# Kernel optimization log

Hardware: AMD Instinct MI355X
Metric: run time of the kernel (lower is better)

The kernel has to match this reference:

```python
import jax, jax.numpy as jnp
import numpy as np
from jax import lax

C = 64      # embed_dim
DI = 128    # d_inner (expand=2)
N = 16      # d_state
RK = 4      # dt_rank = ceil(C/16)
K = 4       # scan directions
NB = 8      # total VSS blocks (4 stages x 2)


def conv2d(x, w, b, stride=1, pad=1, groups=1):
    y = lax.conv_general_dilated(x, w, (stride, stride), [(pad, pad), (pad, pad)],
                                 dimension_numbers=('NCHW', 'OIHW', 'NCHW'),
                                 feature_group_count=groups)
    return y + b[None, :, None, None]


def ln2d(x, g, b, eps=1e-6):
    xt = x.transpose(0, 2, 3, 1)
    mu = xt.mean(-1, keepdims=True)
    var = ((xt - mu) ** 2).mean(-1, keepdims=True)
    y = (xt - mu) / jnp.sqrt(var + eps) * g + b
    return y.transpose(0, 3, 1, 2)


def selective_scan(u, delta, A, Bm, Cm, D):
    # u, delta: (B,K,d,L); A: (K,d,n); Bm, Cm: (B,K,n,L); D: (K,d)
    dA = jnp.exp(delta[..., None] * A[None, :, :, None, :])               # (B,K,d,L,n)
    dBu = delta[..., None] * Bm.transpose(0, 1, 3, 2)[:, :, None] * u[..., None]

    def comb(c1, c2):
        a1, b1 = c1
        a2, b2 = c2
        return a2 * a1, a2 * b1 + b2

    _, h = lax.associative_scan(comb, (dA, dBu), axis=3)                  # (B,K,d,L,n)
    y = jnp.einsum('bkdln,bkln->bkdl', h, Cm.transpose(0, 1, 3, 2))
    return y + D[None, :, :, None] * u


def vss_block(x, lg, lb, inw, cw, cb, xpw, dtw, dtb, a_log, dp, ong, onb, outw):
    B, _, H, W = x.shape
    L = H * W
    h = ln2d(x, lg, lb)
    xz = jnp.einsum('bchw,ce->behw', h, inw)                              # (B,2*DI,H,W)
    xc, z = xz[:, :DI], xz[:, DI:]
    xc = jax.nn.silu(conv2d(xc, cw, cb, groups=DI))                       # depthwise 3x3
    x1 = xc.reshape(B, DI, L)                                             # row-major
    x2 = xc.transpose(0, 1, 3, 2).reshape(B, DI, L)                       # col-major
    xs = jnp.stack([x1, x2, x1[..., ::-1], x2[..., ::-1]], axis=1)        # (B,K,DI,L)
    xdbl = jnp.einsum('bkdl,krd->bkrl', xs, xpw)
    dts, Bs, Cs = xdbl[:, :, :RK], xdbl[:, :, RK:RK + N], xdbl[:, :, RK + N:]
    delta = jax.nn.softplus(jnp.einsum('bkrl,kdr->bkdl', dts, dtw) + dtb[None, :, :, None])
    A = -jnp.exp(a_log)
    ys = selective_scan(xs, delta, A, Bs, Cs, dp)                         # (B,K,DI,L)
    y = (ys[:, 0].reshape(B, DI, H, W)
         + ys[:, 1].reshape(B, DI, W, H).transpose(0, 1, 3, 2)
         + ys[:, 2, :, ::-1].reshape(B, DI, H, W)
         + ys[:, 3, :, ::-1].reshape(B, DI, W, H).transpose(0, 1, 3, 2))
    yt = y.transpose(0, 2, 3, 1)
    mu = yt.mean(-1, keepdims=True)
    var = ((yt - mu) ** 2).mean(-1, keepdims=True)
    yt = (yt - mu) / jnp.sqrt(var + 1e-6) * ong + onb
    yt = yt * jax.nn.silu(z.transpose(0, 2, 3, 1))
    out = jnp.einsum('bhwd,dc->bhwc', yt, outw).transpose(0, 3, 1, 2)
    return x + out


def setup_inputs() -> dict:
    key = jax.random.key(0)
    ks = jax.random.split(key, 16)
    nrm = lambda k, s, sc=0.02: jax.random.normal(k, s, jnp.float32) * sc
    return dict(
        E0=jax.random.uniform(ks[0], (1, 1, 256, 256), jnp.float32),
        pe_w=nrm(ks[1], (C, 1, 4, 4), 0.1),
        pe_b=jnp.zeros((C,), jnp.float32),
        pe_lg=jnp.ones((C,), jnp.float32),
        pe_lb=jnp.zeros((C,), jnp.float32),
        ln_g=jnp.ones((NB, C), jnp.float32),
        ln_b=jnp.zeros((NB, C), jnp.float32),
        in_w=nrm(ks[2], (NB, C, 2 * DI)),
        cv_w=nrm(ks[3], (NB, DI, 1, 3, 3), 0.1),
        cv_b=jnp.zeros((NB, DI), jnp.float32),
        xp_w=nrm(ks[4], (NB, K, RK + 2 * N, DI)),
        dt_w=nrm(ks[5], (NB, K, DI, RK)),
        dt_b=nrm(ks[6], (NB, K, DI), 0.5),
        A_log=jnp.broadcast_to(jnp.log(jnp.arange(1., N + 1)), (NB, K, DI, N)).astype(jnp.float32),
        Dp=jnp.ones((NB, K, DI), jnp.float32),
        on_g=jnp.ones((NB, DI), jnp.float32),
        on_b=jnp.zeros((NB, DI), jnp.float32),
        out_pw=nrm(ks[7], (NB, DI, C)),
        dn_w=nrm(ks[8], (3, C, C, 3, 3), 0.05),
        dn_b=jnp.zeros((3, C), jnp.float32),
        dn_g=jnp.ones((3, C), jnp.float32),
        dn_lb=jnp.zeros((3, C), jnp.float32),
        up_w=nrm(ks[9], (3, C, C, 3, 3), 0.05),
        up_b=jnp.zeros((3, C), jnp.float32),
        oc_w=nrm(ks[10], (C, C, 3, 3), 0.05),
        oc_b=jnp.zeros((C,), jnp.float32),
    )


def reference(E0, pe_w, pe_b, pe_lg, pe_lb, ln_g, ln_b, in_w, cv_w, cv_b, xp_w,
              dt_w, dt_b, A_log, Dp, on_g, on_b, out_pw, dn_w, dn_b, dn_g, dn_lb,
              up_w, up_b, oc_w, oc_b):
    x = conv2d(E0, pe_w, pe_b, stride=4, pad=0)
    x = ln2d(x, pe_lg, pe_lb)
    skips = []
    cur = 0
    for i in range(4):
        for _ in range(2):
            x = vss_block(x, ln_g[cur], ln_b[cur], in_w[cur], cv_w[cur], cv_b[cur],
                          xp_w[cur], dt_w[cur], dt_b[cur], A_log[cur], Dp[cur],
                          on_g[cur], on_b[cur], out_pw[cur])
            cur += 1
        skips.append(x)
        if i < 3:
            x = ln2d(conv2d(x, dn_w[i], dn_b[i], stride=2), dn_g[i], dn_lb[i])
    for i in range(3):
        Bq, Cq, Hq, Wq = x.shape
        x = jax.image.resize(x, (Bq, Cq, Hq * 2, Wq * 2), method='bilinear')
        x = jax.nn.silu(conv2d(x, up_w[i], up_b[i]))
        x = x + skips[-(i + 2)]
    Bq, Cq, Hq, Wq = x.shape
    x = jax.image.resize(x, (Bq, Cq, Hq * 4, Wq * 4), method='bilinear')
    x = jax.nn.silu(conv2d(x, oc_w, oc_b))
    return x
```

## Files before the change

### kernel.cpp

```cpp
#include <hip/hip_runtime.h>
#include <hip/hip_bf16.h>
#include <utility>

__global__ void k_patch_embed_ln(const float* __restrict__ E0, const float* __restrict__ w,
                                 const float* __restrict__ b, const float* __restrict__ g,
                                 const float* __restrict__ lb, float* __restrict__ out) {
  int p = blockIdx.x;
  int c = threadIdx.x;
  int oh = p >> 6, ow = p & 63;
  const float* src = E0 + (oh * 4) * 256 + ow * 4;
  const float* wc = w + c * 16;
  float acc = b[c];
#pragma unroll
  for (int i = 0; i < 4; i++)
#pragma unroll
    for (int j = 0; j < 4; j++) acc += src[i * 256 + j] * wc[i * 4 + j];
  float s = acc, s2 = acc * acc;
#pragma unroll
  for (int m = 32; m >= 1; m >>= 1) {
    s += __shfl_xor(s, m, 64);
    s2 += __shfl_xor(s2, m, 64);
  }
  float mu = s * (1.f / 64.f);
  float var = s2 * (1.f / 64.f) - mu * mu;
  float rstd = rsqrtf(var + 1e-6f);
  out[c * 4096 + p] = (acc - mu) * rstd * g[c] + lb[c];
}

__global__ void k_ln2d64(const float* __restrict__ x, const float* __restrict__ g,
                         const float* __restrict__ b, float* __restrict__ y, int HW) {
  int p = blockIdx.x;
  int c = threadIdx.x;
  float v = x[c * HW + p];
  float s = v, s2 = v * v;
#pragma unroll
  for (int m = 32; m >= 1; m >>= 1) {
    s += __shfl_xor(s, m, 64);
    s2 += __shfl_xor(s2, m, 64);
  }
  float mu = s * (1.f / 64.f);
  float var = s2 * (1.f / 64.f) - mu * mu;
  float rstd = rsqrtf(var + 1e-6f);
  y[c * HW + p] = (v - mu) * rstd * g[c] + b[c];
}

__global__ void k_lnproj(const float* __restrict__ x, const float* __restrict__ g,
                         const float* __restrict__ b, const float* __restrict__ w,
                         float* __restrict__ xc, float* __restrict__ z, int HW) {
  int p = blockIdx.x;
  int t = threadIdx.x;
  __shared__ float hsh[64];
  if (t < 64) {
    float v = x[t * HW + p];
    float s = v, s2 = v * v;
#pragma unroll
    for (int m = 32; m >= 1; m >>= 1) {
      s += __shfl_xor(s, m, 64);
      s2 += __shfl_xor(s2, m, 64);
    }
    float mu = s * (1.f / 64.f);
    float var = s2 * (1.f / 64.f) - mu * mu;
    float rstd = rsqrtf(var + 1e-6f);
    hsh[t] = (v - mu) * rstd * g[t] + b[t];
  }
  __syncthreads();
  float acc = 0.f;
  const float* wp = w + t;
#pragma unroll
  for (int c = 0; c < 64; c++) acc += hsh[c] * wp[c * 256];
  if (t < 128)
    xc[(size_t)p * 128 + t] = acc;
  else
    z[(size_t)p * 128 + (t - 128)] = acc;
}

__global__ void k_dwconv(const float* __restrict__ xc, const float* __restrict__ w,
                         const float* __restrict__ b, float* __restrict__ out, int H, int lgH) {
  int HW = H * H;
  int idx = blockIdx.x * blockDim.x + threadIdx.x;
  if (idx >= 128 * HW) return;
  int p = idx >> 7;
  int d = idx & 127;
  int ph = p >> lgH, pw = p & (H - 1);
  const float* wp = w + d * 9;
  float acc = b[d];
#pragma unroll
  for (int i = 0; i < 3; i++) {
    int ih = ph + i - 1;
    if (ih < 0 || ih >= H) continue;
#pragma unroll
    for (int j = 0; j < 3; j++) {
      int iw = pw + j - 1;
      if (iw < 0 || iw >= H) continue;
      acc += xc[(size_t)(ih * H + iw) * 128 + d] * wp[i * 3 + j];
    }
  }
  out[(size_t)p * 128 + d] = acc / (1.f + __expf(-acc));
}

__global__ void __launch_bounds__(256) k_xproj_scanA(
    const float* __restrict__ xcs, const float* __restrict__ xpw,
    const float* __restrict__ dtw, const float* __restrict__ dtb,
    const float* __restrict__ A_log, float* __restrict__ delta, float* __restrict__ Bs,
    float* __restrict__ Cs, float* __restrict__ hloc, float* __restrict__ pA, int H,
    int lgH, int nc, int cs) {
  int L = H * H;
  int c = blockIdx.x;
  int k = blockIdx.y;
  int t = threadIdx.x;
  int l0 = c * cs;
  __shared__ float xs[32][128];
  __shared__ float dsh[32][128];
  __shared__ float Bsh[32][16];
  __shared__ float r4s[4];
  for (int i = t; i < cs * 128; i += 256) {
    int j = i >> 7, d = i & 127;
    int l = l0 + j;
    int lm = (k & 2) ? (L - 1 - l) : l;
    int idx = (k & 1) ? ((lm & (H - 1)) * H + (lm >> lgH)) : lm;
    xs[j][d] = xcs[(size_t)idx * 128 + d];
  }
  int r = t >> 2, q = t & 3;
  float4 wreg[8];
  if (t < 144) {
    const float4* wp = (const float4*)(xpw + (size_t)(k * 36 + r) * 128 + q * 32);
#pragma unroll
    for (int m = 0; m < 8; m++) wreg[m] = wp[m];
  }
  float4 dtw4 = {0, 0, 0, 0};
  float dtbv = 0.f;
  if (t < 128) {
    dtw4 = *(const float4*)(dtw + (size_t)(k * 128 + t) * 4);
    dtbv = dtb[k * 128 + t];
  }
  __syncthreads();
  for (int j = 0; j < cs; j++) {
    if (t < 144) {
      const float4* xp = (const float4*)&xs[j][q * 32];
      float a = 0.f;
#pragma unroll
      for (int m = 0; m < 8; m++) {
        float4 xv = xp[m];
        a += xv.x * wreg[m].x + xv.y * wreg[m].y + xv.z * wreg[m].z + xv.w * wreg[m].w;
      }
      a += __shfl_xor(a, 1);
      a += __shfl_xor(a, 2);
      if (q == 0) {
        int l = l0 + j;
        if (r < 4)
          r4s[r] = a;
        else if (r < 20) {
          Bsh[j][r - 4] = a;
          Bs[((size_t)k * L + l) * 16 + (r - 4)] = a;
        } else
          Cs[((size_t)k * L + l) * 16 + (r - 20)] = a;
      }
    }
    __syncthreads();
    if (t < 128) {
      float dt = dtbv + r4s[0] * dtw4.x + r4s[1] * dtw4.y + r4s[2] * dtw4.z + r4s[3] * dtw4.w;
      float sp = fmaxf(dt, 0.f) + log1pf(__expf(-fabsf(dt)));
      dsh[j][t] = sp;
      delta[((size_t)k * L + (l0 + j)) * 128 + t] = sp;
    }
    __syncthreads();
  }
  if (t < 128) {
    int d = t;
    float A[16], h[16];
#pragma unroll
    for (int n = 0; n < 16; n++) {
      A[n] = -__expf(A_log[(size_t)(k * 128 + d) * 16 + n]);
      h[n] = 0.f;
    }
    float sumdt = 0.f;
    for (int j = 0; j < cs; j++) {
      float u = xs[j][d];
      float dt = dsh[j][d];
      float du = dt * u;
      sumdt += dt;
      const float4* bp = (const float4*)Bsh[j];
      float4 B0 = bp[0], B1 = bp[1], B2 = bp[2], B3 = bp[3];
      float Bv[16] = {B0.x, B0.y, B0.z, B0.w, B1.x, B1.y, B1.z, B1.w,
                      B2.x, B2.y, B2.z, B2.w, B3.x, B3.y, B3.z, B3.w};
#pragma unroll
      for (int n = 0; n < 16; n++) h[n] = __expf(dt * A[n]) * h[n] + Bv[n] * du;
    }
    size_t base = (((size_t)(k * 128 + d)) * nc + c) * 16;
#pragma unroll
    for (int n = 0; n < 16; n++) {
      hloc[base + n] = h[n];
      pA[base + n] = __expf(A[n] * sumdt);
    }
  }
}

__global__ void k_scanB(const float* __restrict__ hloc, const float* __restrict__ pA,
                        float* __restrict__ hinit, int nc) {
  int tid = blockIdx.x * blockDim.x + threadIdx.x;
  int k = tid >> 11;
  int d = (tid >> 4) & 127;
  int n = tid & 15;
  size_t rb = ((size_t)(k * 128 + d)) * nc * 16 + n;
  float h = 0.f;
  for (int c = 0; c < nc; c++) {
    size_t a = rb + (size_t)c * 16;
    hinit[a] = h;
    h = pA[a] * h + hloc[a];
  }
}

__global__ void k_scanC(const float* __restrict__ xcs, const float* __restrict__ delta,
                        const float* __restrict__ Bs, const float* __restrict__ Cs,
                        const float* __restrict__ A_log, const float* __restrict__ Dp,
                        const float* __restrict__ hinit, float* __restrict__ ys, int H,
                        int lgH, int nc, int cs) {
  int L = H * H;
  int c = blockIdx.x;
  int k = blockIdx.y;
  int d = threadIdx.x;
  float A[16], h[16];
  size_t base = (((size_t)(k * 128 + d)) * nc + c) * 16;
#pragma unroll
  for (int n = 0; n < 16; n++) {
    A[n] = -__expf(A_log[(size_t)(k * 128 + d) * 16 + n]);
    h[n] = hinit[base + n];
  }
  float Dv = Dp[k * 128 + d];
  int l0 = c * cs;
  for (int l = l0; l < l0 + cs; l++) {
    int lm = (k & 2) ? (L - 1 - l) : l;
    int idx = (k & 1) ? ((lm & (H - 1)) * H + (lm >> lgH)) : lm;
    float u = xcs[(size_t)idx * 128 + d];
    float dt = delta[((size_t)k * L + l) * 128 + d];
    float du = dt * u;
    const float4* bp = (const float4*)(Bs + ((size_t)k * L + l) * 16);
    float4 B0 = bp[0], B1 = bp[1], B2 = bp[2], B3 = bp[3];
    float Bv[16] = {B0.x, B0.y, B0.z, B0.w, B1.x, B1.y, B1.z, B1.w,
                    B2.x, B2.y, B2.z, B2.w, B3.x, B3.y, B3.z, B3.w};
    const float4* cp = (const float4*)(Cs + ((size_t)k * L + l) * 16);
    float4 C0 = cp[0], C1 = cp[1], C2 = cp[2], C3 = cp[3];
    float Cv[16] = {C0.x, C0.y, C0.z, C0.w, C1.x, C1.y, C1.z, C1.w,
                    C2.x, C2.y, C2.z, C2.w, C3.x, C3.y, C3.z, C3.w};
    float y = 0.f;
#pragma unroll
    for (int n = 0; n < 16; n++) {
      h[n] = __expf(dt * A[n]) * h[n] + Bv[n] * du;
      y += h[n] * Cv[n];
    }
    ys[((size_t)k * L + l) * 128 + d] = y + Dv * u;
  }
}

__global__ void k_combine(const float* __restrict__ ys, const float* __restrict__ z,
                          const float* __restrict__ xin, const float* __restrict__ ong,
                          const float* __restrict__ onb, const float* __restrict__ outw,
                          float* __restrict__ xout, int H, int lgH) {
  int L = H * H;
  int p = blockIdx.x;
  int d = threadIdx.x;
  int ph = p >> lgH, pw = p & (H - 1);
  int l1 = pw * H + ph;
  float yv = ys[((size_t)0 * L + p) * 128 + d] + ys[((size_t)1 * L + l1) * 128 + d] +
             ys[((size_t)2 * L + (L - 1 - p)) * 128 + d] +
             ys[((size_t)3 * L + (L - 1 - l1)) * 128 + d];
  float s = yv, s2 = yv * yv;
#pragma unroll
  for (int m = 32; m >= 1; m >>= 1) {
    s += __shfl_xor(s, m, 64);
    s2 += __shfl_xor(s2, m, 64);
  }
  __shared__ float ws1[2], ws2[2];
  int wid = d >> 6;
  if ((d & 63) == 0) {
    ws1[wid] = s;
    ws2[wid] = s2;
  }
  __syncthreads();
  float tot = ws1[0] + ws1[1], tot2 = ws2[0] + ws2[1];
  float mu = tot * (1.f / 128.f);
  float var = tot2 * (1.f / 128.f) - mu * mu;
  float rstd = rsqrtf(var + 1e-6f);
  float zt = z[(size_t)p * 128 + d];
  float yt = ((yv - mu) * rstd * ong[d] + onb[d]) * (zt / (1.f + __expf(-zt)));
  __shared__ float ysm[128];
  ysm[d] = yt;
  __syncthreads();
  if (d < 64) {
    float acc = xin[(size_t)d * L + p];
#pragma unroll
    for (int q = 0; q < 128; q++) acc += ysm[q] * outw[q * 64 + d];
    xout[(size_t)d * L + p] = acc;
  }
}

__global__ void k_combine_lnproj(const float* __restrict__ ys, const float* __restrict__ z,
                                 const float* __restrict__ xin, const float* __restrict__ ong,
                                 const float* __restrict__ onb, const float* __restrict__ outw,
                                 const float* __restrict__ g2, const float* __restrict__ b2,
                                 const float* __restrict__ w2, float* __restrict__ xout,
                                 float* __restrict__ xc, float* __restrict__ zout, int H,
                                 int lgH) {
  int L = H * H;
  int p = blockIdx.x;
  int t = threadIdx.x;
  __shared__ float ysm[128], hnsh[64];
  __shared__ float ws1[2], ws2[2];
  float yv = 0.f;
  if (t < 128) {
    int ph = p >> lgH, pw = p & (H - 1);
    int l1 = pw * H + ph;
    yv = ys[((size_t)0 * L + p) * 128 + t] + ys[((size_t)1 * L + l1) * 128 + t] +
         ys[((size_t)2 * L + (L - 1 - p)) * 128 + t] +
         ys[((size_t)3 * L + (L - 1 - l1)) * 128 + t];
    float s = yv, s2 = yv * yv;
#pragma unroll
    for (int m = 32; m >= 1; m >>= 1) {
      s += __shfl_xor(s, m, 64);
      s2 += __shfl_xor(s2, m, 64);
    }
    if ((t & 63) == 0) {
      ws1[t >> 6] = s;
      ws2[t >> 6] = s2;
    }
  }
  __syncthreads();
  if (t < 128) {
    float tot = ws1[0] + ws1[1], tot2 = ws2[0] + ws2[1];
    float mu = tot * (1.f / 128.f);
    float var = tot2 * (1.f / 128.f) - mu * mu;
    float rstd = rsqrtf(var + 1e-6f);
    float zt = z[(size_t)p * 128 + t];
    ysm[t] = ((yv - mu) * rstd * ong[t] + onb[t]) * (zt / (1.f + __expf(-zt)));
  }
  __syncthreads();
  if (t < 64) {
    float acc = xin[(size_t)t * L + p];
#pragma unroll
    for (int q = 0; q < 128; q++) acc += ysm[q] * outw[q * 64 + t];
    xout[(size_t)t * L + p] = acc;
    float s = acc, s2 = acc * acc;
#pragma unroll
    for (int m = 32; m >= 1; m >>= 1) {
      s += __shfl_xor(s, m, 64);
      s2 += __shfl_xor(s2, m, 64);
    }
    float mu = s * (1.f / 64.f);
    float var = s2 * (1.f / 64.f) - mu * mu;
    float rstd = rsqrtf(var + 1e-6f);
    hnsh[t] = (acc - mu) * rstd * g2[t] + b2[t];
  }
  __syncthreads();
  float a2 = 0.f;
  const float* wp = w2 + t;
#pragma unroll
  for (int c = 0; c < 64; c++) a2 += hnsh[c] * wp[c * 256];
  if (t < 128)
    xc[(size_t)p * 128 + t] = a2;
  else
    zout[(size_t)p * 128 + (t - 128)] = a2;
}

__global__ void k_conv_naive(const float* __restrict__ x, const float* __restrict__ w,
                             const float* __restrict__ b, const float* __restrict__ skip,
                             float* __restrict__ out, int Hin, int Hout, int stride,
                             int do_silu) {
  int idx = blockIdx.x * blockDim.x + threadIdx.x;
  int HWo = Hout * Hout;
  if (idx >= 64 * HWo) return;
  int co = idx / HWo;
  int p = idx - co * HWo;
  int oh = p / Hout, ow = p - (p / Hout) * Hout;
  float acc = b[co];
  const float* wb = w + co * 64 * 9;
  for (int ci = 0; ci < 64; ci++) {
    const float* xb = x + (size_t)ci * Hin * Hin;
    const float* wc = wb + ci * 9;
#pragma unroll
    for (int i = 0; i < 3; i++) {
      int ih = oh * stride + i - 1;
      if (ih < 0 || ih >= Hin) continue;
#pragma unroll
      for (int j = 0; j < 3; j++) {
        int iw = ow * stride + j - 1;
        if (iw < 0 || iw >= Hin) continue;
        acc += xb[ih * Hin + iw] * wc[i * 3 + j];
      }
    }
  }
  if (do_silu) acc = acc / (1.f + __expf(-acc));
  if (skip) acc += skip[idx];
  out[idx] = acc;
}

__global__ void __launch_bounds__(256) k_conv16_up(const float* __restrict__ x,
                                                   const float* __restrict__ w,
                                                   const float* __restrict__ b,
                                                   float* __restrict__ out) {
  __shared__ float ssh[64][36];
  __shared__ float pfh[324], pfw[324];
  __shared__ int poff[324];
  __shared__ __align__(16) float xsh[8][18][20];
  __shared__ __align__(16) float wsh[8][32][12];
  int t = threadIdx.x;
  int q = t & 63, cog = t >> 6;
  int qx = q & 7, qy = q >> 3;
  int ox = blockIdx.x * 16, oy = blockIdx.y * 16;
  int z32 = blockIdx.z * 32;
  int sy0 = (oy >> 2) - 1, sx0 = (ox >> 2) - 1;
  for (int i = t; i < 64 * 36; i += 256) {
    int ci = i / 36;
    int rr = i - ci * 36;
    int ry = rr / 6, cc = rr - ry * 6;
    int sy = min(max(sy0 + ry, 0), 63);
    int sx = min(max(sx0 + cc, 0), 63);
    ssh[ci][rr] = x[(size_t)ci * 4096 + sy * 64 + sx];
  }
  for (int i = t; i < 324; i += 256) {
    int iy = i / 18, ix = i - iy * 18;
    int gy = oy + iy - 1, gx = ox + ix - 1;
    if ((unsigned)gy < 256u && (unsigned)gx < 256u) {
      float sh = gy * 0.25f - 0.375f;
      float sw = gx * 0.25f - 0.375f;
      int h0 = (int)floorf(sh), w0 = (int)floorf(sw);
      pfh[i] = sh - h0;
      pfw[i] = sw - w0;
      poff[i] = (h0 - sy0) * 6 + (w0 - sx0);
    } else {
      poff[i] = -1;
      pfh[i] = 0.f;
      pfw[i] = 0.f;
    }
  }
  float acc[4][8];
#pragma unroll
  for (int pp = 0; pp < 4; pp++)
#pragma unroll
    for (int i = 0; i < 8; i++) acc[pp][i] = 0.f;
  __syncthreads();
  for (int cb = 0; cb < 64; cb += 8) {
    for (int i = t; i < 8 * 324; i += 256) {
      int ci = i / 324;
      int rdx = i - ci * 324;
      int off = poff[rdx];
      float v = 0.f;
      if (off >= 0) {
        float fh = pfh[rdx], fw = pfw[rdx];
        const float* s = &ssh[cb + ci][off];
        v = (1.f - fh) * ((1.f - fw) * s[0] + fw * s[1]) +
            fh * ((1.f - fw) * s[6] + fw * s[7]);
      }
      int iy = rdx / 18;
      xsh[ci][iy][rdx - iy * 18] = v;
    }
    for (int i = t; i < 8 * 288; i += 256) {
      int ci = i / 288;
      int rr = i - ci * 288;
      int col = rr / 9, tap = rr - col * 9;
      wsh[ci][col][tap] = w[(size_t)(z32 + col) * 576 + (cb + ci) * 9 + tap];
    }
    __syncthreads();
#pragma unroll
    for (int ci = 0; ci < 8; ci++) {
      float xv[4][4];
#pragma unroll
      for (int r = 0; r < 4; r++) {
        float2 a = *(const float2*)&xsh[ci][2 * qy + r][2 * qx];
        float2 bq = *(const float2*)&xsh[ci][2 * qy + r][2 * qx + 2];
        xv[r][0] = a.x;
        xv[r][1] = a.y;
        xv[r][2] = bq.x;
        xv[r][3] = bq.y;
      }
#pragma unroll
      for (int i = 0; i < 8; i++) {
        int col = cog * 8 + i;
        float4 w0v = *(const float4*)&wsh[ci][col][0];
        float4 w1v = *(const float4*)&wsh[ci][col][4];
        float w8v = wsh[ci][col][8];
#pragma unroll
        for (int dy = 0; dy < 2; dy++)
#pragma unroll
          for (int dx = 0; dx < 2; dx++) {
            acc[dy * 2 + dx][i] += xv[dy + 0][dx + 0] * w0v.x + xv[dy + 0][dx + 1] * w0v.y +
                                   xv[dy + 0][dx + 2] * w0v.z + xv[dy + 1][dx + 0] * w0v.w +
                                   xv[dy + 1][dx + 1] * w1v.x + xv[dy + 1][dx + 2] * w1v.y +
                                   xv[dy + 2][dx + 0] * w1v.z + xv[dy + 2][dx + 1] * w1v.w +
                                   xv[dy + 2][dx + 2] * w8v;
          }
      }
    }
    __syncthreads();
  }
#pragma unroll
  for (int dy = 0; dy < 2; dy++)
#pragma unroll
    for (int dx = 0; dx < 2; dx++) {
      int gy = oy + 2 * qy + dy, gx = ox + 2 * qx + dx;
#pragma unroll
      for (int i = 0; i < 8; i++) {
        int co = z32 + cog * 8 + i;
        float a = acc[dy * 2 + dx][i] + b[co];
        a = a / (1.f + __expf(-a));
        out[(size_t)co * 65536 + gy * 256 + gx] = a;
      }
    }
}

__global__ void k_resize(const float* __restrict__ x, float* __restrict__ out, int Hin,
                         int Win, int Hout, int Wout, float inv_scale) {
  int idx = blockIdx.x * blockDim.x + threadIdx.x;
  int HWo = Hout * Wout;
  if (idx >= 64 * HWo) return;
  int c = idx / HWo;
  int p = idx - c * HWo;
  int oh = p / Wout, ow = p - (p / Wout) * Wout;
  float sh = (oh + 0.5f) * inv_scale - 0.5f;
  float sw = (ow + 0.5f) * inv_scale - 0.5f;
  int h0 = (int)floorf(sh);
  float fh = sh - h0;
  int w0 = (int)floorf(sw);
  float fw = sw - w0;
  int h0c = min(max(h0, 0), Hin - 1), h1c = min(max(h0 + 1, 0), Hin - 1);
  int w0c = min(max(w0, 0), Win - 1), w1c = min(max(w0 + 1, 0), Win - 1);
  const float* xb = x + (size_t)c * Hin * Win;
  float v = (1.f - fh) * ((1.f - fw) * xb[h0c * Win + w0c] + fw * xb[h0c * Win + w1c]) +
            fh * ((1.f - fw) * xb[h1c * Win + w0c] + fw * xb[h1c * Win + w1c]);
  out[idx] = v;
}

extern "C" void kernel_launch(void* const* d_in, const int* in_sizes, int n_in, void* d_out,
                              int out_size, void* d_ws, size_t ws_size, hipStream_t stream) {
  const float* E0 = (const float*)d_in[0];
  const float* pe_w = (const float*)d_in[1];
  const float* pe_b = (const float*)d_in[2];
  const float* pe_lg = (const float*)d_in[3];
  const float* pe_lb = (const float*)d_in[4];
  const float* ln_g = (const float*)d_in[5];
  const float* ln_b = (const float*)d_in[6];
  const float* in_w = (const float*)d_in[7];
  const float* cv_w = (const float*)d_in[8];
  const float* cv_b = (const float*)d_in[9];
  const float* xp_w = (const float*)d_in[10];
  const float* dt_w = (const float*)d_in[11];
  const float* dt_b = (const float*)d_in[12];
  const float* A_log = (const float*)d_in[13];
  const float* Dp = (const float*)d_in[14];
  const float* on_g = (const float*)d_in[15];
  const float* on_b = (const float*)d_in[16];
  const float* out_pw = (const float*)d_in[17];
  const float* dn_w = (const float*)d_in[18];
  const float* dn_b = (const float*)d_in[19];
  const float* dn_g = (const float*)d_in[20];
  const float* dn_lb = (const float*)d_in[21];
  const float* up_w = (const float*)d_in[22];
  const float* up_b = (const float*)d_in[23];
  const float* oc_w = (const float*)d_in[24];
  const float* oc_b = (const float*)d_in[25];

  float* ws = (float*)d_ws;
  size_t off = 0;
  auto alloc = [&](size_t n) {
    float* p = ws + off;
    off += n;
    return p;
  };
  float* xA = alloc(64 * 4096);
  float* xB = alloc(64 * 4096);
  float* xc = alloc(128 * 4096);
  float* zb = alloc(128 * 4096);
  float* xcs = alloc(128 * 4096);
  float* dlt = alloc((size_t)4 * 128 * 4096);
  float* Bsb = alloc(4 * 16 * 4096);
  float* Csb = alloc(4 * 16 * 4096);
  float* ysb = alloc((size_t)4 * 128 * 4096);
  float* hloc = alloc((size_t)4 * 128 * 128 * 16);
  float* pAb = alloc((size_t)4 * 128 * 128 * 16);
  float* hin = alloc((size_t)4 * 128 * 128 * 16);
  float* sk0 = alloc(64 * 4096);
  float* sk1 = alloc(64 * 1024);
  float* sk2 = alloc(64 * 256);
  float* sk3 = alloc(64 * 64);
  float* tmpR = alloc((size_t)64 * 4096);

  k_patch_embed_ln<<<4096, 64, 0, stream>>>(E0, pe_w, pe_b, pe_lg, pe_lb, xB);
  float* x = xB;
  float* xalt = xA;

  int Hs[4] = {64, 32, 16, 8};
  int lgHs[4] = {6, 5, 4, 3};
  int CSs[4] = {32, 16, 8, 8};
  float* skips[4] = {sk0, sk1, sk2, sk3};
  int cur = 0;

  auto vss_core = [&](int H, int lgH, int cs) {
    int L = H * H;
    int nc = L / cs;
    k_dwconv<<<(128 * L + 255) / 256, 256, 0, stream>>>(xc, cv_w + (size_t)cur * 128 * 9,
                                                        cv_b + cur * 128, xcs, H, lgH);
    const float* Al = A_log + (size_t)cur * 4 * 128 * 16;
    const float* Dv = Dp + cur * 4 * 128;
    dim3 ga(nc, 4);
    k_xproj_scanA<<<ga, 256, 0, stream>>>(xcs, xp_w + (size_t)cur * 4 * 36 * 128,
                                          dt_w + (size_t)cur * 4 * 128 * 4,
                                          dt_b + cur * 4 * 128, Al, dlt, Bsb, Csb, hloc,
                                          pAb, H, lgH, nc, cs);
    k_scanB<<<32, 256, 0, stream>>>(hloc, pAb, hin, nc);
    dim3 gc(nc, 4);
    k_scanC<<<gc, 128, 0, stream>>>(xcs, dlt, Bsb, Csb, Al, Dv, hin, ysb, H, lgH, nc, cs);
  };

  for (int i = 0; i < 4; i++) {
    int H = Hs[i], lgH = lgHs[i];
    int L = H * H;
    k_lnproj<<<L, 256, 0, stream>>>(x, ln_g + cur * 64, ln_b + cur * 64,
                                    in_w + (size_t)cur * 64 * 256, xc, zb, L);
    vss_core(H, lgH, CSs[i]);
    k_combine_lnproj<<<L, 256, 0, stream>>>(
        ysb, zb, x, on_g + cur * 128, on_b + cur * 128, out_pw + (size_t)cur * 128 * 64,
        ln_g + (cur + 1) * 64, ln_b + (cur + 1) * 64, in_w + (size_t)(cur + 1) * 64 * 256,
        xalt, xc, zb, H, lgH);
    std::swap(x, xalt);
    cur++;
    vss_core(H, lgH, CSs[i]);
    if (i < 3) {
      k_combine<<<L, 128, 0, stream>>>(ysb, zb, x, on_g + cur * 128, on_b + cur * 128,
                                       out_pw + (size_t)cur * 128 * 64, skips[i], H, lgH);
      cur++;
      int Ho = H / 2;
      k_conv_naive<<<(64 * Ho * Ho + 255) / 256, 256, 0, stream>>>(
          skips[i], dn_w + (size_t)i * 64 * 64 * 9, dn_b + i * 64, nullptr, xalt, H, Ho, 2, 0);
      k_ln2d64<<<Ho * Ho, 64, 0, stream>>>(xalt, dn_g + i * 64, dn_lb + i * 64, x, Ho * Ho);
    } else {
      k_combine<<<L, 128, 0, stream>>>(ysb, zb, x, on_g + cur * 128, on_b + cur * 128,
                                       out_pw + (size_t)cur * 128 * 64, xalt, H, lgH);
      std::swap(x, xalt);
      cur++;
    }
  }

  for (int i = 0; i < 3; i++) {
    int Hin = 8 << i, Ho = Hin * 2;
    k_resize<<<(64 * Ho * Ho + 255) / 256, 256, 0, stream>>>(x, tmpR, Hin, Hin, Ho, Ho, 0.5f);
    k_conv_naive<<<(64 * Ho * Ho + 255) / 256, 256, 0, stream>>>(
        tmpR, up_w + (size_t)i * 64 * 64 * 9, up_b + i * 64, skips[2 - i], xalt, Ho, Ho, 1, 1);
    std::swap(x, xalt);
  }

  dim3 gf(16, 16, 2);
  k_conv16_up<<<gf, 256, 0, stream>>>(x, oc_w, oc_b, (float*)d_out);
}
```

Baseline: 1.230 ms.

## Fold bilinear 4x upsample into phase-decomposed conv weights for final layer

The final 4x bilinear upsample plus 3x3 conv is rewritten as 16 polyphase 3x3 convolutions applied directly on the 64x64 input, using weights pre-combined with the interpolation coefficients. The per-block bilinear interpolation of the input tile in shared memory goes away, as does most of the redundant work on the upsampled grid. Border pixels, where clamping breaks the phase identity, are recomputed by a separate ring kernel. This adds a weight-prep kernel and an extra launch, and the interior results are overwritten by the ring kernel only at image edges.

```diff
diff --git a/kernel.cpp b/kernel.cpp
--- a/kernel.cpp
+++ b/kernel.cpp
@@ -393,71 +393,95 @@
   out[idx] = acc;
 }
 
-__global__ void __launch_bounds__(256) k_conv16_up(const float* __restrict__ x,
-                                                   const float* __restrict__ w,
-                                                   const float* __restrict__ b,
-                                                   float* __restrict__ out) {
-  __shared__ float ssh[64][36];
-  __shared__ float pfh[324], pfw[324];
-  __shared__ int poff[324];
-  __shared__ __align__(16) float xsh[8][18][20];
-  __shared__ __align__(16) float wsh[8][32][12];
+__global__ void k_phase_weights(const float* __restrict__ w, float* __restrict__ Wp) {
+  int co = blockIdx.x;
+  int ph = blockIdx.y;
+  int ci = threadIdx.x;
+  int py = ph >> 2, px = ph & 3;
+  float ay[3][3], ax[3][3];
+#pragma unroll
+  for (int d = 0; d < 3; d++)
+#pragma unroll
+    for (int s = 0; s < 3; s++) {
+      ay[d][s] = 0.f;
+      ax[d][s] = 0.f;
+    }
+#pragma unroll
+  for (int d = 0; d < 3; d++) {
+    {
+      float tt = (py + d - 1) * 0.25f - 0.375f;
+      float e = floorf(tt);
+      float f = tt - e;
+      int ei = (int)e;
+#pragma unroll
+      for (int s = 0; s < 3; s++) {
+        if (s == ei + 1) ay[d][s] += 1.f - f;
+        if (s == ei + 2) ay[d][s] += f;
+      }
+    }
+    {
+      float tt = (px + d - 1) * 0.25f - 0.375f;
+      float e = floorf(tt);
+      float f = tt - e;
+      int ei = (int)e;
+#pragma unroll
+      for (int s = 0; s < 3; s++) {
+        if (s == ei + 1) ax[d][s] += 1.f - f;
+        if (s == ei + 2) ax[d][s] += f;
+      }
+    }
+  }
+  const float* wc = w + ((size_t)co * 64 + ci) * 9;
+  float wv[9];
+#pragma unroll
+  for (int i = 0; i < 9; i++) wv[i] = wc[i];
+  float* dst = Wp + (((size_t)ph * 64 + co) * 64 + ci) * 9;
+#pragma unroll
+  for (int sy = 0; sy < 3; sy++)
+#pragma unroll
+    for (int sx = 0; sx < 3; sx++) {
+      float a = 0.f;
+#pragma unroll
+      for (int dy = 0; dy < 3; dy++)
+#pragma unroll
+        for (int dx = 0; dx < 3; dx++) a += wv[dy * 3 + dx] * ay[dy][sy] * ax[dx][sx];
+      dst[sy * 3 + sx] = a;
+    }
+}
+
+__global__ void __launch_bounds__(256) k_conv_phase(const float* __restrict__ x,
+                                                    const float* __restrict__ Wp,
+                                                    const float* __restrict__ bias,
+                                                    float* __restrict__ out) {
+  __shared__ __align__(16) float ssh[8][18][20];
+  __shared__ __align__(16) float wsh[8][16][12];
   int t = threadIdx.x;
-  int q = t & 63, cog = t >> 6;
+  int q = t & 63, cg = t >> 6;
   int qx = q & 7, qy = q >> 3;
-  int ox = blockIdx.x * 16, oy = blockIdx.y * 16;
-  int z32 = blockIdx.z * 32;
-  int sy0 = (oy >> 2) - 1, sx0 = (ox >> 2) - 1;
-  for (int i = t; i < 64 * 36; i += 256) {
-    int ci = i / 36;
-    int rr = i - ci * 36;
-    int ry = rr / 6, cc = rr - ry * 6;
-    int sy = min(max(sy0 + ry, 0), 63);
-    int sx = min(max(sx0 + cc, 0), 63);
-    ssh[ci][rr] = x[(size_t)ci * 4096 + sy * 64 + sx];
-  }
-  for (int i = t; i < 324; i += 256) {
-    int iy = i / 18, ix = i - iy * 18;
-    int gy = oy + iy - 1, gx = ox + ix - 1;
-    if ((unsigned)gy < 256u && (unsigned)gx < 256u) {
-      float sh = gy * 0.25f - 0.375f;
-      float sw = gx * 0.25f - 0.375f;
-      int h0 = (int)floorf(sh), w0 = (int)floorf(sw);
-      pfh[i] = sh - h0;
-      pfw[i] = sw - w0;
-      poff[i] = (h0 - sy0) * 6 + (w0 - sx0);
-    } else {
-      poff[i] = -1;
-      pfh[i] = 0.f;
-      pfw[i] = 0.f;
-    }
-  }
-  float acc[4][8];
+  int tx = blockIdx.x & 3, ty = blockIdx.x >> 2;
+  int ph = blockIdx.y;
+  int py = ph >> 2, px = ph & 3;
+  int z16 = blockIdx.z * 16;
+  int by = ty * 16, bx = tx * 16;
+  float acc[4][4];
 #pragma unroll
   for (int pp = 0; pp < 4; pp++)
 #pragma unroll
-    for (int i = 0; i < 8; i++) acc[pp][i] = 0.f;
-  __syncthreads();
+    for (int i = 0; i < 4; i++) acc[pp][i] = 0.f;
   for (int cb = 0; cb < 64; cb += 8) {
     for (int i = t; i < 8 * 324; i += 256) {
       int ci = i / 324;
-      int rdx = i - ci * 324;
-      int off = poff[rdx];
-      float v = 0.f;
-      if (off >= 0) {
-        float fh = pfh[rdx], fw = pfw[rdx];
-        const float* s = &ssh[cb + ci][off];
-        v = (1.f - fh) * ((1.f - fw) * s[0] + fw * s[1]) +
-            fh * ((1.f - fw) * s[6] + fw * s[7]);
-      }
-      int iy = rdx / 18;
-      xsh[ci][iy][rdx - iy * 18] = v;
-    }
-    for (int i = t; i < 8 * 288; i += 256) {
-      int ci = i / 288;
-      int rr = i - ci * 288;
+      int rr = i - ci * 324;
+      int ry = rr / 18, rx = rr - ry * 18;
+      int sy = min(max(by + ry - 1, 0), 63);
+      int sx = min(max(bx + rx - 1, 0), 63);
+      ssh[ci][ry][rx] = x[(size_t)(cb + ci) * 4096 + sy * 64 + sx];
+    }
+    for (int i = t; i < 8 * 144; i += 256) {
+      int ci = i / 144;
+      int rr = i - ci * 144;
       int col = rr / 9, tap = rr - col * 9;
-      wsh[ci][col][tap] = w[(size_t)(z32 + col) * 576 + (cb + ci) * 9 + tap];
+      wsh[ci][col][tap] = Wp[(((size_t)ph * 64 + z16 + col) * 64 + cb + ci) * 9 + tap];
     }
     __syncthreads();
 #pragma unroll
@@ -465,46 +489,112 @@
       float xv[4][4];
 #pragma unroll
       for (int r = 0; r < 4; r++) {
-        float2 a = *(const float2*)&xsh[ci][2 * qy + r][2 * qx];
-        float2 bq = *(const float2*)&xsh[ci][2 * qy + r][2 * qx + 2];
+        float2 a = *(const float2*)&ssh[ci][2 * qy + r][2 * qx];
+        float2 bq = *(const float2*)&ssh[ci][2 * qy + r][2 * qx + 2];
         xv[r][0] = a.x;
         xv[r][1] = a.y;
         xv[r][2] = bq.x;
         xv[r][3] = bq.y;
       }
 #pragma unroll
-      for (int i = 0; i < 8; i++) {
-        int col = cog * 8 + i;
-        float4 w0v = *(const float4*)&wsh[ci][col][0];
-        float4 w1v = *(const float4*)&wsh[ci][col][4];
-        float w8v = wsh[ci][col][8];
-#pragma unroll
-        for (int dy = 0; dy < 2; dy++)
-#pragma unroll
-          for (int dx = 0; dx < 2; dx++) {
-            acc[dy * 2 + dx][i] += xv[dy + 0][dx + 0] * w0v.x + xv[dy + 0][dx + 1] * w0v.y +
-                                   xv[dy + 0][dx + 2] * w0v.z + xv[dy + 1][dx + 0] * w0v.w +
-                                   xv[dy + 1][dx + 1] * w1v.x + xv[dy + 1][dx + 2] * w1v.y +
-                                   xv[dy + 2][dx + 0] * w1v.z + xv[dy + 2][dx + 1] * w1v.w +
-                                   xv[dy + 2][dx + 2] * w8v;
+      for (int i = 0; i < 4; i++) {
+        int col = cg * 4 + i;
+        float4 w0 = *(const float4*)&wsh[ci][col][0];
+        float4 w1 = *(const float4*)&wsh[ci][col][4];
+        float w8 = wsh[ci][col][8];
+#pragma unroll
+        for (int dr = 0; dr < 2; dr++)
+#pragma unroll
+          for (int dc = 0; dc < 2; dc++) {
+            acc[dr * 2 + dc][i] += xv[dr + 0][dc + 0] * w0.x + xv[dr + 0][dc + 1] * w0.y +
+                                   xv[dr + 0][dc + 2] * w0.z + xv[dr + 1][dc + 0] * w0.w +
+                                   xv[dr + 1][dc + 1] * w1.x + xv[dr + 1][dc + 2] * w1.y +
+                                   xv[dr + 2][dc + 0] * w1.z + xv[dr + 2][dc + 1] * w1.w +
+                                   xv[dr + 2][dc + 2] * w8;
           }
       }
     }
     __syncthreads();
   }
 #pragma unroll
-  for (int dy = 0; dy < 2; dy++)
-#pragma unroll
-    for (int dx = 0; dx < 2; dx++) {
-      int gy = oy + 2 * qy + dy, gx = ox + 2 * qx + dx;
-#pragma unroll
-      for (int i = 0; i < 8; i++) {
-        int co = z32 + cog * 8 + i;
-        float a = acc[dy * 2 + dx][i] + b[co];
+  for (int dr = 0; dr < 2; dr++)
+#pragma unroll
+    for (int dc = 0; dc < 2; dc++) {
+      int sy = by + 2 * qy + dr, sx = bx + 2 * qx + dc;
+      int gy = 4 * sy + py, gx = 4 * sx + px;
+#pragma unroll
+      for (int i = 0; i < 4; i++) {
+        int co = z16 + cg * 4 + i;
+        float a = acc[dr * 2 + dc][i] + bias[co];
         a = a / (1.f + __expf(-a));
         out[(size_t)co * 65536 + gy * 256 + gx] = a;
       }
     }
+}
+
+__global__ void k_final_ring(const float* __restrict__ x, const float* __restrict__ w,
+                             const float* __restrict__ b, float* __restrict__ out) {
+  int tid = blockIdx.x * blockDim.x + threadIdx.x;
+  if (tid >= 1020 * 64) return;
+  int co = tid & 63;
+  int pix = tid >> 6;
+  int gy, gx;
+  if (pix < 256) {
+    gy = 0;
+    gx = pix;
+  } else if (pix < 512) {
+    gy = 255;
+    gx = pix - 256;
+  } else if (pix < 766) {
+    gy = pix - 512 + 1;
+    gx = 0;
+  } else {
+    gy = pix - 766 + 1;
+    gx = 255;
+  }
+  float fh[3], fw[3];
+  int y0[3], y1[3], x0[3], x1[3];
+  bool vy[3], vx[3];
+#pragma unroll
+  for (int d = 0; d < 3; d++) {
+    int g = gy + d - 1;
+    vy[d] = (g >= 0 && g < 256);
+    float s = g * 0.25f - 0.375f;
+    float e = floorf(s);
+    int ei = (int)e;
+    fh[d] = s - e;
+    y0[d] = min(max(ei, 0), 63);
+    y1[d] = min(max(ei + 1, 0), 63);
+    g = gx + d - 1;
+    vx[d] = (g >= 0 && g < 256);
+    s = g * 0.25f - 0.375f;
+    e = floorf(s);
+    ei = (int)e;
+    fw[d] = s - e;
+    x0[d] = min(max(ei, 0), 63);
+    x1[d] = min(max(ei + 1, 0), 63);
+  }
+  const float* wb = w + (size_t)co * 576;
+  float acc = b[co];
+  for (int ci = 0; ci < 64; ci++) {
+    const float* xb = x + (size_t)ci * 4096;
+    const float* wc = wb + ci * 9;
+#pragma unroll
+    for (int dy = 0; dy < 3; dy++) {
+      if (!vy[dy]) continue;
+#pragma unroll
+      for (int dx = 0; dx < 3; dx++) {
+        if (!vx[dx]) continue;
+        float u = (1.f - fh[dy]) * ((1.f - fw[dx]) * xb[y0[dy] * 64 + x0[dx]] +
+                                    fw[dx] * xb[y0[dy] * 64 + x1[dx]]) +
+                  fh[dy] * ((1.f - fw[dx]) * xb[y1[dy] * 64 + x0[dx]] +
+                            fw[dx] * xb[y1[dy] * 64 + x1[dx]]);
+        acc += wc[dy * 3 + dx] * u;
+      }
+    }
+  }
+  acc = acc / (1.f + __expf(-acc));
+  out[(size_t)co * 65536 + gy * 256 + gx] = acc;
 }
 
 __global__ void k_resize(const float* __restrict__ x, float* __restrict__ out, int Hin,
@@ -582,6 +672,9 @@
   float* sk2 = alloc(64 * 256);
   float* sk3 = alloc(64 * 64);
   float* tmpR = alloc((size_t)64 * 4096);
+  float* Wpb = alloc((size_t)16 * 64 * 64 * 9);
+
+  k_phase_weights<<<dim3(64, 16), 64, 0, stream>>>(oc_w, Wpb);
 
   k_patch_embed_ln<<<4096, 64, 0, stream>>>(E0, pe_w, pe_b, pe_lg, pe_lb, xB);
   float* x = xB;
@@ -647,6 +740,7 @@
     std::swap(x, xalt);
   }
 
-  dim3 gf(16, 16, 2);
-  k_conv16_up<<<gf, 256, 0, stream>>>(x, oc_w, oc_b, (float*)d_out);
-}
+  dim3 gp(16, 16, 4);
+  k_conv_phase<<<gp, 256, 0, stream>>>(x, Wpb, oc_b, (float*)d_out);
+  k_final_ring<<<255, 256, 0, stream>>>(x, oc_w, oc_b, (float*)d_out);
+}
```

Result: slower. 1.388 ms (+12.9%).
